# Performance work log

Hardware: AMD Instinct MI355X
Metric: run time of the kernel (lower is better)

## Reference

```python
import jax, jax.numpy as jnp
import numpy as np

VOCAB = 30000
N_NODES = 10000
N_EDGES = 160000
D = 1024


def setup_inputs() -> dict:
    key = jax.random.key(0)
    ks = jax.random.split(key, 10)
    s = 1.0 / np.sqrt(D)
    return {
        "node": jax.random.randint(ks[0], (N_NODES,), 0, VOCAB),
        "src": jax.random.randint(ks[1], (N_EDGES,), 0, N_NODES),
        "dst": jax.random.randint(ks[2], (N_EDGES,), 0, N_NODES),
        "emb": jax.random.normal(ks[3], (VOCAB, D), jnp.float32),
        "W1_self": jax.random.uniform(ks[4], (D, D), jnp.float32, -s, s),
        "W1_neigh": jax.random.uniform(ks[5], (D, D), jnp.float32, -s, s),
        "b1": jax.random.uniform(ks[6], (D,), jnp.float32, -s, s),
        "W2_self": jax.random.uniform(ks[7], (D, D), jnp.float32, -s, s),
        "W2_neigh": jax.random.uniform(ks[8], (D, D), jnp.float32, -s, s),
        "b2": jax.random.uniform(ks[9], (D,), jnp.float32, -s, s),
    }


def _sage_conv(h, src, dst, W_self, W_neigh, b):
    # DGL SAGEConv 'mean': mean over in-neighbors (src -> dst), 0 for isolated dst
    n = h.shape[0]
    deg = jax.ops.segment_sum(jnp.ones((src.shape[0],), h.dtype), dst, num_segments=n)
    agg = jax.ops.segment_sum(h[src], dst, num_segments=n)  # [n, D]
    h_neigh = agg / jnp.maximum(deg, 1.0)[:, None]
    # rst = fc_self(h) + fc_neigh(h_neigh); fc_self has no bias in DGL
    return h @ W_self + h_neigh @ W_neigh + b


def reference(node, src, dst, emb, W1_self, W1_neigh, b1, W2_self, W2_neigh, b2):
    x = emb[node]  # [N_NODES, D] embedding lookup
    h = jax.nn.relu(_sage_conv(x, src, dst, W1_self, W1_neigh, b1))
    return _sage_conv(h, src, dst, W2_self, W2_neigh, b2)
```

## Files before the change

### kernel.cpp

```cpp
#include <hip/hip_runtime.h>
#include <hip/hip_bf16.h>

#define N_NODES 10000
#define N_EDGES 160000
#define DD 1024
#define KCAT 2048
#define MPAD 10240
#define MTILES 79
#define NTILES 8
#define NBLK (MTILES * NTILES)
#define NSTEP 64

#define AGG_BLOCKS 2000
#define AGG_WPS 1000

typedef __attribute__((ext_vector_type(8))) __bf16 bf16x8;
typedef __attribute__((ext_vector_type(4))) __bf16 bf16x4;
typedef __attribute__((ext_vector_type(4))) float f32x4;

__device__ inline void gload_lds16(const void* g, void* l) {
  __builtin_amdgcn_global_load_lds((const __attribute__((address_space(1))) void*)g,
                                   (__attribute__((address_space(3))) void*)l, 16, 0, 0);
}

__global__ __launch_bounds__(256) void k_prep1(const int* __restrict__ dst,
                                               int* __restrict__ deg,
                                               const int* __restrict__ node,
                                               const float* __restrict__ emb,
                                               __bf16* __restrict__ xcat) {
  int b = blockIdx.x;
  if (b < 625) {
    int e = b * 256 + threadIdx.x;
    if (e < N_EDGES) atomicAdd(&deg[dst[e]], 1);
  } else {
    int i = b - 625;
    int t = threadIdx.x;
    float4 v = ((const float4*)(emb + (size_t)node[i] * DD))[t];
    bf16x4 o;
    o[0] = (__bf16)v.x; o[1] = (__bf16)v.y; o[2] = (__bf16)v.z; o[3] = (__bf16)v.w;
    *(bf16x4*)(xcat + (size_t)i * KCAT + t * 4) = o;
  }
}

__global__ __launch_bounds__(1024) void k_scan(const int* __restrict__ deg,
                                               int* __restrict__ off) {
  __shared__ int wtot[16];
  __shared__ int wpre[16];
  __shared__ int carry_s;
  int t = threadIdx.x, lane = t & 63, w = t >> 6;
  if (t == 0) carry_s = 0;
  __syncthreads();
  for (int c = 0; c < 10; ++c) {
    int idx = c * 1024 + t;
    int v = (idx < N_NODES) ? deg[idx] : 0;
    int inc = v;
#pragma unroll
    for (int d = 1; d < 64; d <<= 1) {
      int y = __shfl_up(inc, d);
      if (lane >= d) inc += y;
    }
    if (lane == 63) wtot[w] = inc;
    __syncthreads();
    if (t == 0) {
      int acc = carry_s;
      for (int k = 0; k < 16; ++k) { wpre[k] = acc; acc += wtot[k]; }
      carry_s = acc;
    }
    __syncthreads();
    if (idx < N_NODES) off[idx] = wpre[w] + (inc - v);
  }
  if (t == 0) off[N_NODES] = carry_s;
}

__global__ __launch_bounds__(256) void k_prep2(const int* __restrict__ src,
                                               const int* __restrict__ dstv,
                                               const int* __restrict__ off,
                                               int* __restrict__ cursor,
                                               int* __restrict__ eidx,
                                               const float* __restrict__ W1s,
                                               const float* __restrict__ W1n,
                                               const float* __restrict__ W2s,
                                               const float* __restrict__ W2n,
                                               __bf16* __restrict__ Wt1,
                                               __bf16* __restrict__ Wt2) {
  int b = blockIdx.x;
  if (b < 625) {
    int e = b * 256 + threadIdx.x;
    if (e < N_EDGES) {
      int d = dstv[e];
      int pos = atomicAdd(&cursor[d], 1);
      eidx[off[d] + pos] = src[e];
    }
    return;
  }
  int id = b - 625;
  int k0 = (id & 63) * 32;
  int c0 = ((id >> 6) & 31) * 32;
  int lay = id >> 11;
  const float* Ws = lay ? W2s : W1s;
  const float* Wn = lay ? W2n : W1n;
  __bf16* Wt = lay ? Wt2 : Wt1;
  __shared__ float tile[32][33];
  int tx = threadIdx.x & 31, ty = threadIdx.x >> 5;
  for (int i = ty; i < 32; i += 8) {
    int k = k0 + i, c = c0 + tx;
    float v = (k < DD) ? Ws[(size_t)k * DD + c] : Wn[(size_t)(k - DD) * DD + c];
    tile[i][tx] = v;
  }
  __syncthreads();
  for (int i = ty; i < 32; i += 8) {
    int c = c0 + i, k = k0 + tx;
    Wt[(size_t)c * KCAT + k] = (__bf16)tile[tx][i];
  }
}

__global__ __launch_bounds__(256) void k_agg(__bf16* __restrict__ buf,
                                             const int* __restrict__ off,
                                             const int* __restrict__ eidx) {
  const int s    = blockIdx.x & 7;
  const int q    = blockIdx.x >> 3;
  const int lane = threadIdx.x & 63;
  const int w    = threadIdx.x >> 6;
  const int g    = lane >> 4;
  const int l    = lane & 15;
  const int wid  = q * 4 + w;
  const size_t colb = (size_t)s * 128 + l * 8;

  for (int n = wid; n < N_NODES; n += AGG_WPS) {
    const int s0 = off[n], e0 = off[n + 1];
    float acc[8];
#pragma unroll
    for (int j = 0; j < 8; ++j) acc[j] = 0.f;
    int i = s0;
    for (; i + 8 <= e0; i += 8) {
      int eA = eidx[i + g];
      int eB = eidx[i + 4 + g];
      bf16x8 vA = *(const bf16x8*)(buf + (size_t)eA * KCAT + colb);
      bf16x8 vB = *(const bf16x8*)(buf + (size_t)eB * KCAT + colb);
#pragma unroll
      for (int j = 0; j < 8; ++j) acc[j] += (float)vA[j] + (float)vB[j];
    }
    if (i + 4 <= e0) {
      int eA = eidx[i + g];
      bf16x8 vA = *(const bf16x8*)(buf + (size_t)eA * KCAT + colb);
#pragma unroll
      for (int j = 0; j < 8; ++j) acc[j] += (float)vA[j];
      i += 4;
    }
    int rem = e0 - i;
    if (g < rem) {
      int eA = eidx[i + g];
      bf16x8 vA = *(const bf16x8*)(buf + (size_t)eA * KCAT + colb);
#pragma unroll
      for (int j = 0; j < 8; ++j) acc[j] += (float)vA[j];
    }
#pragma unroll
    for (int j = 0; j < 8; ++j) {
      acc[j] += __shfl_xor(acc[j], 16);
      acc[j] += __shfl_xor(acc[j], 32);
    }
    if (g == 0) {
      float inv = 1.0f / fmaxf((float)(e0 - s0), 1.0f);
      bf16x8 o;
#pragma unroll
      for (int j = 0; j < 8; ++j) o[j] = (__bf16)(acc[j] * inv);
      *(bf16x8*)(buf + (size_t)n * KCAT + DD + colb) = o;
    }
  }
}

template <int MODE>
__global__ __launch_bounds__(256, 3) void k_gemm(const __bf16* __restrict__ A,
                                                 const __bf16* __restrict__ Bt,
                                                 const float* __restrict__ bias,
                                                 float* __restrict__ Cf,
                                                 __bf16* __restrict__ Cb,
                                                 int Mreal) {
  __shared__ char smem[49152];
  const int tid  = threadIdx.x;
  const int lane = tid & 63;
  const int w    = tid >> 6;
  const int wr   = w >> 1, wc = w & 1;
  const int b  = blockIdx.x;
  const int l  = (b & 7) * MTILES + (b >> 3);
  const int m0 = (l >> 3) * 128;
  const int n0 = (l & 7) * 128;

  f32x4 acc[4][4];
#pragma unroll
  for (int m = 0; m < 4; ++m)
#pragma unroll
    for (int n = 0; n < 4; ++n) acc[m][n] = f32x4{0.f, 0.f, 0.f, 0.f};

  int srow[2], sko[2];
#pragma unroll
  for (int i = 0; i < 2; ++i) {
    int G = i * 256 + tid;
    srow[i] = G >> 2;
    sko[i] = ((G & 3) ^ ((srow[i] >> 1) & 3)) * 8;
  }

  auto stage = [&](int buf, int kt) {
    char* Ab = smem + buf * 16384;
    char* Bb = Ab + 8192;
#pragma unroll
    for (int i = 0; i < 2; ++i) {
      gload_lds16(A + (size_t)(m0 + srow[i]) * KCAT + (kt + sko[i]), Ab + i * 4096 + w * 1024);
      gload_lds16(Bt + (size_t)(n0 + srow[i]) * KCAT + (kt + sko[i]), Bb + i * 4096 + w * 1024);
    }
  };

  auto compute = [&](int buf) {
    char* Ab = smem + buf * 16384;
    char* Bb = Ab + 8192;
    const int c = lane >> 4;
    bf16x8 af[4], bfr[4];
#pragma unroll
    for (int m = 0; m < 4; ++m) {
      int r = wr * 64 + m * 16 + (lane & 15);
      af[m] = *(const bf16x8*)(Ab + r * 64 + ((c ^ ((r >> 1) & 3)) << 4));
    }
#pragma unroll
    for (int n = 0; n < 4; ++n) {
      int r = wc * 64 + n * 16 + (lane & 15);
      bfr[n] = *(const bf16x8*)(Bb + r * 64 + ((c ^ ((r >> 1) & 3)) << 4));
    }
#pragma unroll
    for (int m = 0; m < 4; ++m)
#pragma unroll
      for (int n = 0; n < 4; ++n)
        acc[m][n] = __builtin_amdgcn_mfma_f32_16x16x32_bf16(af[m], bfr[n], acc[m][n], 0, 0, 0);
  };

  stage(0, 0);
  stage(1, 32);
  int cur = 0, nxt = 2;
  for (int t = 0; t < NSTEP; ++t) {
    if (t + 2 < NSTEP) {
      stage(nxt, (t + 2) * 32);
      asm volatile("s_waitcnt vmcnt(8)" ::: "memory");
    } else if (t + 1 < NSTEP) {
      asm volatile("s_waitcnt vmcnt(4)" ::: "memory");
    } else {
      asm volatile("s_waitcnt vmcnt(0)" ::: "memory");
    }
    __builtin_amdgcn_sched_barrier(0);
    __builtin_amdgcn_s_barrier();
    __builtin_amdgcn_sched_barrier(0);
    compute(cur);
    __builtin_amdgcn_sched_barrier(0);
    __builtin_amdgcn_s_barrier();
    __builtin_amdgcn_sched_barrier(0);
    cur = (cur == 2) ? 0 : cur + 1;
    nxt = (nxt == 2) ? 0 : nxt + 1;
  }

  const int rb = m0 + wr * 64;
  const int cb = n0 + wc * 64;
#pragma unroll
  for (int m = 0; m < 4; ++m) {
#pragma unroll
    for (int n = 0; n < 4; ++n) {
      int cc = cb + n * 16 + (lane & 15);
      float bv = bias[cc];
#pragma unroll
      for (int j = 0; j < 4; ++j) {
        int r = rb + m * 16 + (lane >> 4) * 4 + j;
        if (r < Mreal) {
          float v = acc[m][n][j] + bv;
          if constexpr (MODE == 1) {
            v = fmaxf(v, 0.f);
            Cb[(size_t)r * KCAT + cc] = (__bf16)v;
          } else {
            Cf[(size_t)r * DD + cc] = v;
          }
        }
      }
    }
  }
}

extern "C" void kernel_launch(void* const* d_in, const int* in_sizes, int n_in,
                              void* d_out, int out_size, void* d_ws, size_t ws_size,
                              hipStream_t stream) {
  const int*   node = (const int*)d_in[0];
  const int*   srcv = (const int*)d_in[1];
  const int*   dstv = (const int*)d_in[2];
  const float* emb  = (const float*)d_in[3];
  const float* W1s  = (const float*)d_in[4];
  const float* W1n  = (const float*)d_in[5];
  const float* b1   = (const float*)d_in[6];
  const float* W2s  = (const float*)d_in[7];
  const float* W2n  = (const float*)d_in[8];
  const float* b2   = (const float*)d_in[9];
  float* out = (float*)d_out;

  char* ws = (char*)d_ws;
  __bf16* xcat = (__bf16*)ws; ws += (size_t)MPAD * KCAT * 2;
  __bf16* hcat = (__bf16*)ws; ws += (size_t)MPAD * KCAT * 2;
  __bf16* Wt1  = (__bf16*)ws; ws += (size_t)DD * KCAT * 2;
  __bf16* Wt2  = (__bf16*)ws; ws += (size_t)DD * KCAT * 2;
  int* deg    = (int*)ws; ws += 40960;
  int* cursor = (int*)ws; ws += 40960;
  int* off    = (int*)ws; ws += 40960;
  int* eidx   = (int*)ws; ws += (size_t)N_EDGES * 4;

  hipMemsetAsync(deg, 0, 2 * 40960, stream);

  k_prep1<<<625 + N_NODES, 256, 0, stream>>>(dstv, deg, node, emb, xcat);
  k_scan<<<1, 1024, 0, stream>>>(deg, off);
  k_prep2<<<625 + 4096, 256, 0, stream>>>(srcv, dstv, off, cursor, eidx,
                                          W1s, W1n, W2s, W2n, Wt1, Wt2);

  k_agg<<<AGG_BLOCKS, 256, 0, stream>>>(xcat, off, eidx);
  k_gemm<1><<<NBLK, 256, 0, stream>>>(xcat, Wt1, b1, nullptr, hcat, N_NODES);

  k_agg<<<AGG_BLOCKS, 256, 0, stream>>>(hcat, off, eidx);
  k_gemm<0><<<NBLK, 256, 0, stream>>>(hcat, Wt2, b2, out, nullptr, N_NODES);
}
```

Before: 415.4 us.

## Restructure GEMM to 256x256 tiles with 512 threads and double-buffered 64-wide K

Replaces the 128x128 tile GEMM (632 blocks, 256 threads, triple-buffered K=32) with 256x256 tiles (160 blocks, 512 threads, 8 waves) and double-buffered K=64 stages in 128KB LDS. Loads for the next K-step are interleaved across four sub-phases of the compute, and MFMA sections are wrapped in s_setprio. The larger tile raises arithmetic intensity per LDS byte, but 160 blocks on a GPU with many CUs may leave CUs idle. The 40-row M padding also wastes work at the tail, and per-phase barriers add sync cost.

```diff
diff --git a/kernel.cpp b/kernel.cpp
--- a/kernel.cpp
+++ b/kernel.cpp
@@ -6,10 +6,8 @@
 #define DD 1024
 #define KCAT 2048
 #define MPAD 10240
-#define MTILES 79
-#define NTILES 8
-#define NBLK (MTILES * NTILES)
-#define NSTEP 64
+#define NKT 32
+#define GBLK 160
 
 #define AGG_BLOCKS 2000
 #define AGG_WPS 1000
@@ -170,95 +168,112 @@
 }
 
 template <int MODE>
-__global__ __launch_bounds__(256, 3) void k_gemm(const __bf16* __restrict__ A,
+__global__ __launch_bounds__(512, 2) void k_gemm(const __bf16* __restrict__ A,
                                                  const __bf16* __restrict__ Bt,
                                                  const float* __restrict__ bias,
                                                  float* __restrict__ Cf,
                                                  __bf16* __restrict__ Cb,
                                                  int Mreal) {
-  __shared__ char smem[49152];
+  __shared__ char smem[131072];
   const int tid  = threadIdx.x;
   const int lane = tid & 63;
   const int w    = tid >> 6;
-  const int wr   = w >> 1, wc = w & 1;
-  const int b  = blockIdx.x;
-  const int l  = (b & 7) * MTILES + (b >> 3);
-  const int m0 = (l >> 3) * 128;
-  const int n0 = (l & 7) * 128;
-
-  f32x4 acc[4][4];
-#pragma unroll
-  for (int m = 0; m < 4; ++m)
+  const int wr   = w >> 2;
+  const int wc   = w & 3;
+  const int b    = blockIdx.x;
+  const int l    = (b & 7) * 20 + (b >> 3);
+  const int m0   = (l >> 2) * 256;
+  const int n0   = (l & 3) * 256;
+
+  f32x4 acc[8][4];
+#pragma unroll
+  for (int m = 0; m < 8; ++m)
 #pragma unroll
     for (int n = 0; n < 4; ++n) acc[m][n] = f32x4{0.f, 0.f, 0.f, 0.f};
 
-  int srow[2], sko[2];
-#pragma unroll
-  for (int i = 0; i < 2; ++i) {
-    int G = i * 256 + tid;
-    srow[i] = G >> 2;
-    sko[i] = ((G & 3) ^ ((srow[i] >> 1) & 3)) * 8;
-  }
-
-  auto stage = [&](int buf, int kt) {
-    char* Ab = smem + buf * 16384;
-    char* Bb = Ab + 8192;
-#pragma unroll
-    for (int i = 0; i < 2; ++i) {
-      gload_lds16(A + (size_t)(m0 + srow[i]) * KCAT + (kt + sko[i]), Ab + i * 4096 + w * 1024);
-      gload_lds16(Bt + (size_t)(n0 + srow[i]) * KCAT + (kt + sko[i]), Bb + i * 4096 + w * 1024);
-    }
+  auto stage_round = [&](char* dstbase, const __bf16* S, int gbase, int kt, int i) {
+    int G   = i * 512 + tid;
+    int row = G >> 3;
+    int cc  = (G & 7) ^ (row & 7);
+    gload_lds16(S + (size_t)(gbase + row) * KCAT + kt * 64 + cc * 8,
+                dstbase + i * 8192 + w * 1024 + lane * 16);
   };
 
-  auto compute = [&](int buf) {
-    char* Ab = smem + buf * 16384;
-    char* Bb = Ab + 8192;
-    const int c = lane >> 4;
-    bf16x8 af[4], bfr[4];
-#pragma unroll
-    for (int m = 0; m < 4; ++m) {
-      int r = wr * 64 + m * 16 + (lane & 15);
-      af[m] = *(const bf16x8*)(Ab + r * 64 + ((c ^ ((r >> 1) & 3)) << 4));
-    }
-#pragma unroll
-    for (int n = 0; n < 4; ++n) {
-      int r = wc * 64 + n * 16 + (lane & 15);
-      bfr[n] = *(const bf16x8*)(Bb + r * 64 + ((c ^ ((r >> 1) & 3)) << 4));
-    }
-#pragma unroll
-    for (int m = 0; m < 4; ++m)
-#pragma unroll
-      for (int n = 0; n < 4; ++n)
-        acc[m][n] = __builtin_amdgcn_mfma_f32_16x16x32_bf16(af[m], bfr[n], acc[m][n], 0, 0, 0);
-  };
-
-  stage(0, 0);
-  stage(1, 32);
-  int cur = 0, nxt = 2;
-  for (int t = 0; t < NSTEP; ++t) {
-    if (t + 2 < NSTEP) {
-      stage(nxt, (t + 2) * 32);
-      asm volatile("s_waitcnt vmcnt(8)" ::: "memory");
-    } else if (t + 1 < NSTEP) {
-      asm volatile("s_waitcnt vmcnt(4)" ::: "memory");
-    } else {
-      asm volatile("s_waitcnt vmcnt(0)" ::: "memory");
-    }
-    __builtin_amdgcn_sched_barrier(0);
-    __builtin_amdgcn_s_barrier();
-    __builtin_amdgcn_sched_barrier(0);
-    compute(cur);
-    __builtin_amdgcn_sched_barrier(0);
-    __builtin_amdgcn_s_barrier();
-    __builtin_amdgcn_sched_barrier(0);
-    cur = (cur == 2) ? 0 : cur + 1;
-    nxt = (nxt == 2) ? 0 : nxt + 1;
-  }
-
-  const int rb = m0 + wr * 64;
+  char* A0 = smem;
+  {
+#pragma unroll
+    for (int i = 0; i < 4; ++i) stage_round(A0, A, m0, 0, i);
+#pragma unroll
+    for (int i = 0; i < 4; ++i) stage_round(A0 + 32768, Bt, n0, 0, i);
+  }
+  asm volatile("s_waitcnt vmcnt(0)" ::: "memory");
+  __builtin_amdgcn_sched_barrier(0);
+  __builtin_amdgcn_s_barrier();
+  __builtin_amdgcn_sched_barrier(0);
+
+  for (int kt = 0; kt < NKT; ++kt) {
+    char* Abuf  = smem + (kt & 1) * 65536;
+    char* Bbuf  = Abuf + 32768;
+    char* AbufN = smem + ((kt & 1) ^ 1) * 65536;
+    char* BbufN = AbufN + 32768;
+    bf16x8 bfr[4][2];
+#pragma unroll
+    for (int p = 0; p < 4; ++p) {
+      bf16x8 af[2][2];
+#pragma unroll
+      for (int i = 0; i < 2; ++i)
+#pragma unroll
+        for (int kk = 0; kk < 2; ++kk) {
+          int row = wr * 128 + (2 * p + i) * 16 + (lane & 15);
+          int c   = kk * 4 + (lane >> 4);
+          af[i][kk] = *(const bf16x8*)(Abuf + row * 128 + ((c ^ (row & 7)) << 4));
+        }
+      if (p == 0) {
+#pragma unroll
+        for (int nf = 0; nf < 4; ++nf)
+#pragma unroll
+          for (int kk = 0; kk < 2; ++kk) {
+            int row = wc * 64 + nf * 16 + (lane & 15);
+            int c   = kk * 4 + (lane >> 4);
+            bfr[nf][kk] = *(const bf16x8*)(Bbuf + row * 128 + ((c ^ (row & 7)) << 4));
+          }
+      }
+      if (kt + 1 < NKT) {
+        if (p == 0) {
+#pragma unroll
+          for (int i = 0; i < 4; ++i) stage_round(AbufN, A, m0, kt + 1, i);
+        } else if (p == 1) {
+#pragma unroll
+          for (int i = 0; i < 4; ++i) stage_round(BbufN, Bt, n0, kt + 1, i);
+        }
+      }
+      if (p == 3) {
+        asm volatile("s_waitcnt vmcnt(0)" ::: "memory");
+      }
+      __builtin_amdgcn_sched_barrier(0);
+      __builtin_amdgcn_s_barrier();
+      asm volatile("s_waitcnt lgkmcnt(0)" ::: "memory");
+      __builtin_amdgcn_sched_barrier(0);
+      __builtin_amdgcn_s_setprio(1);
+#pragma unroll
+      for (int i = 0; i < 2; ++i)
+#pragma unroll
+        for (int nf = 0; nf < 4; ++nf)
+#pragma unroll
+          for (int kk = 0; kk < 2; ++kk)
+            acc[2 * p + i][nf] = __builtin_amdgcn_mfma_f32_16x16x32_bf16(
+                af[i][kk], bfr[nf][kk], acc[2 * p + i][nf], 0, 0, 0);
+      __builtin_amdgcn_s_setprio(0);
+      __builtin_amdgcn_sched_barrier(0);
+      __builtin_amdgcn_s_barrier();
+      __builtin_amdgcn_sched_barrier(0);
+    }
+  }
+
+  const int rb = m0 + wr * 128;
   const int cb = n0 + wc * 64;
 #pragma unroll
-  for (int m = 0; m < 4; ++m) {
+  for (int m = 0; m < 8; ++m) {
 #pragma unroll
     for (int n = 0; n < 4; ++n) {
       int cc = cb + n * 16 + (lane & 15);
@@ -313,8 +328,8 @@
                                           W1s, W1n, W2s, W2n, Wt1, Wt2);
 
   k_agg<<<AGG_BLOCKS, 256, 0, stream>>>(xcat, off, eidx);
-  k_gemm<1><<<NBLK, 256, 0, stream>>>(xcat, Wt1, b1, nullptr, hcat, N_NODES);
+  k_gemm<1><<<GBLK, 512, 0, stream>>>(xcat, Wt1, b1, nullptr, hcat, N_NODES);
 
   k_agg<<<AGG_BLOCKS, 256, 0, stream>>>(hcat, off, eidx);
-  k_gemm<0><<<NBLK, 256, 0, stream>>>(hcat, Wt2, b2, out, nullptr, N_NODES);
-}
+  k_gemm<0><<<GBLK, 512, 0, stream>>>(hcat, Wt2, b2, out, nullptr, N_NODES);
+}
```

After: 417.7 us. About the same (+0.6%).
